# Kernel tuning notes

Hardware: AMD Instinct MI355X
Metric: run time of the kernel (lower is better)

Reference implementation:

```python
import jax, jax.numpy as jnp
import numpy as np

TEMPERATURE = 0.5
EPS = 1e-12  # F.normalize eps


def setup_inputs() -> dict:
    key = jax.random.key(0)
    z = jax.random.normal(key, (2048, 8, 256), dtype=jnp.float32)
    return {"z": z}


def reference(z):
    B, D = z.shape[0], z.shape[1]
    z = z.reshape(B, D, -1)  # [B, D, F]
    # F.normalize along features
    norm = jnp.linalg.norm(z, axis=-1, keepdims=True)
    zn = z / jnp.maximum(norm, EPS)

    # Positive term: per sample b, sim among D views -> [B, D, D], off-diagonal sum
    sim_pos = jnp.exp(jnp.einsum('bdf,bef->bde', zn, zn) / TEMPERATURE)
    eye_d = jnp.eye(D, dtype=bool)
    pos = jnp.sum(jnp.where(eye_d[None], 0.0, sim_pos), axis=(1, 2))  # [B]

    # Negative term: per view d, sim among B samples -> [D, B, B], row-wise off-diag mean, summed over views
    sim_neg = jnp.exp(jnp.einsum('bdf,cdf->dbc', zn, zn) / TEMPERATURE)
    eye_b = jnp.eye(B, dtype=bool)
    neg = jnp.sum(jnp.where(eye_b[None], 0.0, sim_neg), axis=-1) / (B - 1)  # [D, B]
    neg = jnp.sum(neg, axis=0)  # [B]

    logits = pos / (pos + neg)  # [B]
    # torch CrossEntropyLoss(reduction='sum') with 1-D input [C] and float target ones(C):
    # loss = -sum_c target_c * log_softmax(logits)_c = -sum(log_softmax(logits))
    error = -jnp.sum(jax.nn.log_softmax(logits))
    return error / B
```

## Files before the change

kernel.cpp:

```cpp
#include <hip/hip_runtime.h>
#include <hip/hip_bf16.h>

#define B_N 2048
#define D_V 8
#define F_D 256
#define TILE 128
#define BC 64
#define LSTR 264

#define SCALE_F 1.69864364f

#if defined(__has_builtin)
#  if __has_builtin(__builtin_amdgcn_exp2f)
#    define EXP2F(x) __builtin_amdgcn_exp2f(x)
#  else
#    define EXP2F(x) exp2f(x)
#  endif
#else
#  define EXP2F(x) exp2f(x)
#endif

typedef __attribute__((ext_vector_type(8))) short short8;
typedef __attribute__((ext_vector_type(4))) float floatx4;

__device__ inline unsigned short f2bf(float f) {
    __hip_bfloat16 h = __float2bfloat16(f);
    return *reinterpret_cast<unsigned short*>(&h);
}

__device__ inline float wave_reduce_sum(float v) {
    #pragma unroll
    for (int off = 1; off < 64; off <<= 1)
        v += __shfl_xor(v, off, 64);
    return v;
}

__device__ inline float wave_reduce_max(float v) {
    #pragma unroll
    for (int off = 1; off < 64; off <<= 1)
        v = fmaxf(v, __shfl_xor(v, off, 64));
    return v;
}

__global__ __launch_bounds__(256)
void np_kernel(const float* __restrict__ z, unsigned short* __restrict__ zn,
               float* __restrict__ ns8, float* __restrict__ pos) {
    __shared__ __align__(16) unsigned short Zs[32 * LSTR];
    int tid = threadIdx.x;
    int gid = blockIdx.x * 256 + tid;
    if (gid < D_V * B_N) ns8[gid] = 0.0f;

    int w = tid >> 6, lane = tid & 63;
    int b = blockIdx.x * 4 + w;
    #pragma unroll
    for (int k = 0; k < 8; k++) {
        const float4 v = ((const float4*)(z + ((size_t)b * 8 + k) * F_D))[lane];
        float ss = v.x * v.x + v.y * v.y + v.z * v.z + v.w * v.w;
        ss = wave_reduce_sum(ss);
        float inv = SCALE_F / fmaxf(sqrtf(ss), 1e-12f);
        ushort4 o;
        o.x = f2bf(v.x * inv);
        o.y = f2bf(v.y * inv);
        o.z = f2bf(v.z * inv);
        o.w = f2bf(v.w * inv);
        ((ushort4*)(zn + (size_t)k * (B_N * F_D) + (size_t)b * F_D))[lane] = o;
        *(ushort4*)(&Zs[(w * 8 + k) * LSTR + lane * 4]) = o;
    }
    __syncthreads();

    if (w < 2) {
        int q = lane >> 4, li = lane & 15;
        int lr = (w * 2 + (li >> 3)) * 8 + (li & 7);
        short8 a[8];
        #pragma unroll
        for (int kk = 0; kk < 8; kk++)
            a[kk] = *(const short8*)(&Zs[lr * LSTR + kk * 32 + q * 8]);
        floatx4 acc = {0.f, 0.f, 0.f, 0.f};
        #pragma unroll
        for (int kk = 0; kk < 8; kk++)
            acc = __builtin_amdgcn_mfma_f32_16x16x32_bf16(a[kk], a[kk], acc, 0, 0, 0);
        float p0 = 0.f, p1 = 0.f;
        #pragma unroll
        for (int r = 0; r < 4; r++) {
            int row = q * 4 + r, col = li;
            bool same_sample = (row >> 3) == (col >> 3);
            if (same_sample && row != col) {
                float e = EXP2F(acc[r]);
                if (row < 8) p0 += e; else p1 += e;
            }
        }
        p0 = wave_reduce_sum(p0);
        p1 = wave_reduce_sum(p1);
        if (lane == 0) {
            int s0 = blockIdx.x * 4 + w * 2;
            pos[s0] = p0;
            pos[s0 + 1] = p1;
        }
    }
}

__global__ __launch_bounds__(512)
void neg_kernel(const unsigned short* __restrict__ zn,
                float* __restrict__ ns8) {
    __shared__ __align__(16) unsigned short Bs[BC * LSTR];
    const int bid = blockIdx.x;
    const int d = bid & 7;
    int trem = bid >> 3;
    int i = 0;
    while (trem >= 16 - i) { trem -= 16 - i; ++i; }
    const int j = i + trem;
    const bool diag = (i == j);
    const unsigned short* Z = zn + (size_t)d * (B_N * F_D);
    int tid = threadIdx.x, w = tid >> 6, lane = tid & 63;
    int q = lane >> 4, li = lane & 15;
    int r0 = i * TILE + w * 16;
    const int jc = j * TILE;

    short8 a[8];
    #pragma unroll
    for (int kk = 0; kk < 8; kk++)
        a[kk] = *(const short8*)(Z + (size_t)(r0 + li) * F_D + kk * 32 + q * 8);

    short8 breg[4];
    #pragma unroll
    for (int it = 0; it < 4; ++it) {
        int idx = it * 512 + tid;
        int row = idx >> 5, kc = idx & 31;
        breg[it] = *(const short8*)(Z + (size_t)(jc + row) * F_D + kc * 8);
    }
    #pragma unroll
    for (int it = 0; it < 4; ++it) {
        int idx = it * 512 + tid;
        int row = idx >> 5, kc = idx & 31;
        *(short8*)(&Bs[row * LSTR + kc * 8]) = breg[it];
    }
    #pragma unroll
    for (int it = 0; it < 4; ++it) {
        int idx = it * 512 + tid;
        int row = idx >> 5, kc = idx & 31;
        breg[it] = *(const short8*)(Z + (size_t)(jc + BC + row) * F_D + kc * 8);
    }

    float rs[4] = {0.f, 0.f, 0.f, 0.f};
    float cs[8];

    __syncthreads();

    #pragma unroll
    for (int stage = 0; stage < 2; ++stage) {
        #pragma unroll
        for (int ct = 0; ct < 4; ++ct) {
            const unsigned short* bp = &Bs[(ct * 16 + li) * LSTR + q * 8];
            floatx4 acc = {0.f, 0.f, 0.f, 0.f};
            #pragma unroll
            for (int kk = 0; kk < 8; kk++) {
                short8 bf = *(const short8*)(bp + kk * 32);
                acc = __builtin_amdgcn_mfma_f32_16x16x32_bf16(a[kk], bf, acc, 0, 0, 0);
            }
            int gcol = jc + stage * BC + ct * 16 + li;
            float csum = 0.f;
            #pragma unroll
            for (int r = 0; r < 4; r++) {
                float e = EXP2F(acc[r]);
                if (diag) {
                    int grow = r0 + q * 4 + r;
                    if (grow == gcol) e = 0.f;
                }
                rs[r] += e;
                csum += e;
            }
            csum += __shfl_xor(csum, 16, 64);
            csum += __shfl_xor(csum, 32, 64);
            cs[stage * 4 + ct] = csum;
        }
        if (stage == 0) {
            __syncthreads();
            #pragma unroll
            for (int it = 0; it < 4; ++it) {
                int idx = it * 512 + tid;
                int row = idx >> 5, kc = idx & 31;
                *(short8*)(&Bs[row * LSTR + kc * 8]) = breg[it];
            }
            __syncthreads();
        }
    }

    #pragma unroll
    for (int off = 1; off < 16; off <<= 1)
        #pragma unroll
        for (int r = 0; r < 4; r++)
            rs[r] += __shfl_xor(rs[r], off, 64);
    {
        float rv = 0.f;
        #pragma unroll
        for (int r = 0; r < 4; r++)
            if (li == r) rv = rs[r];
        if (li < 4)
            atomicAdd(&ns8[d * B_N + r0 + q * 4 + li], rv);
    }

    if (!diag) {
        float v0 = 0.f, v1 = 0.f;
        #pragma unroll
        for (int c = 0; c < 4; c++)
            if (q == c) { v0 = cs[c]; v1 = cs[c + 4]; }
        atomicAdd(&ns8[d * B_N + jc + q * 16 + li], v0);
        atomicAdd(&ns8[d * B_N + jc + 64 + q * 16 + li], v1);
    }
}

__global__ void final_kernel(const float* __restrict__ pos,
                             const float* __restrict__ ns8,
                             float* __restrict__ out) {
    __shared__ float redm[4], reds[4], redl[4];
    int t = threadIdx.x, w = t >> 6, lane = t & 63;
    float vals[8];
    float lmax = -1e30f;
    #pragma unroll
    for (int i = 0; i < 8; i++) {
        int idx = t * 8 + i;
        float nsum = 0.f;
        #pragma unroll
        for (int d = 0; d < D_V; d++) nsum += ns8[d * B_N + idx];
        float p = pos[idx];
        float l = p / (p + nsum * (1.0f / (float)(B_N - 1)));
        vals[i] = l;
        lmax = fmaxf(lmax, l);
    }
    lmax = wave_reduce_max(lmax);
    if (lane == 0) redm[w] = lmax;
    __syncthreads();
    float m = fmaxf(fmaxf(redm[0], redm[1]), fmaxf(redm[2], redm[3]));
    float se = 0.f, sl = 0.f;
    #pragma unroll
    for (int i = 0; i < 8; i++) { se += expf(vals[i] - m); sl += vals[i]; }
    se = wave_reduce_sum(se);
    sl = wave_reduce_sum(sl);
    if (lane == 0) { reds[w] = se; redl[w] = sl; }
    __syncthreads();
    if (t == 0) {
        float S = reds[0] + reds[1] + reds[2] + reds[3];
        float L = redl[0] + redl[1] + redl[2] + redl[3];
        out[0] = m + logf(S) - L * (1.0f / (float)B_N);
    }
}

extern "C" void kernel_launch(void* const* d_in, const int* in_sizes, int n_in,
                              void* d_out, int out_size, void* d_ws, size_t ws_size,
                              hipStream_t stream) {
    const float* z = (const float*)d_in[0];
    float* out = (float*)d_out;
    unsigned short* zn = (unsigned short*)d_ws;
    float* ns8 = (float*)((char*)d_ws + (size_t)D_V * B_N * F_D * 2);
    float* pos = ns8 + D_V * B_N;

    np_kernel<<<dim3(512), 256, 0, stream>>>(z, zn, ns8, pos);
    neg_kernel<<<dim3(136 * 8), 512, 0, stream>>>(zn, ns8);
    final_kernel<<<1, 256, 0, stream>>>(pos, ns8, out);
}
```

Baseline: 86.80 us.

## Split neg tiles into row halves and double-buffer B staging in LDS

Each 128x128 tile of the negative-similarity kernel is now handled by two 256-thread blocks, one per 64-row half. The B columns are streamed in four 32-row stages through a two-slot LDS buffer, which needs only one barrier per stage and overlaps the global prefetch with MFMA work. This doubles the number of blocks and lowers LDS use per block, aiming at better occupancy and latency hiding. In exchange, each B tile is loaded twice from global/L2 and twice as many column-sum atomics are issued.

```diff
diff --git a/kernel.cpp b/kernel.cpp
--- a/kernel.cpp
+++ b/kernel.cpp
@@ -5,7 +5,7 @@
 #define D_V 8
 #define F_D 256
 #define TILE 128
-#define BC 64
+#define BC 32
 #define LSTR 264
 
 #define SCALE_F 1.69864364f
@@ -99,13 +99,15 @@
     }
 }
 
-__global__ __launch_bounds__(512)
+__global__ __launch_bounds__(256)
 void neg_kernel(const unsigned short* __restrict__ zn,
                 float* __restrict__ ns8) {
-    __shared__ __align__(16) unsigned short Bs[BC * LSTR];
+    __shared__ __align__(16) unsigned short Bs[2][BC * LSTR];
     const int bid = blockIdx.x;
     const int d = bid & 7;
-    int trem = bid >> 3;
+    int rest = bid >> 3;
+    const int half = rest & 1;
+    int trem = rest >> 1;
     int i = 0;
     while (trem >= 16 - i) { trem -= 16 - i; ++i; }
     const int j = i + trem;
@@ -113,7 +115,7 @@
     const unsigned short* Z = zn + (size_t)d * (B_N * F_D);
     int tid = threadIdx.x, w = tid >> 6, lane = tid & 63;
     int q = lane >> 4, li = lane & 15;
-    int r0 = i * TILE + w * 16;
+    int r0 = i * TILE + half * 64 + w * 16;
     const int jc = j * TILE;
 
     short8 a[8];
@@ -124,19 +126,19 @@
     short8 breg[4];
     #pragma unroll
     for (int it = 0; it < 4; ++it) {
-        int idx = it * 512 + tid;
+        int idx = it * 256 + tid;
         int row = idx >> 5, kc = idx & 31;
         breg[it] = *(const short8*)(Z + (size_t)(jc + row) * F_D + kc * 8);
     }
     #pragma unroll
     for (int it = 0; it < 4; ++it) {
-        int idx = it * 512 + tid;
+        int idx = it * 256 + tid;
         int row = idx >> 5, kc = idx & 31;
-        *(short8*)(&Bs[row * LSTR + kc * 8]) = breg[it];
+        *(short8*)(&Bs[0][row * LSTR + kc * 8]) = breg[it];
     }
     #pragma unroll
     for (int it = 0; it < 4; ++it) {
-        int idx = it * 512 + tid;
+        int idx = it * 256 + tid;
         int row = idx >> 5, kc = idx & 31;
         breg[it] = *(const short8*)(Z + (size_t)(jc + BC + row) * F_D + kc * 8);
     }
@@ -147,17 +149,18 @@
     __syncthreads();
 
     #pragma unroll
-    for (int stage = 0; stage < 2; ++stage) {
-        #pragma unroll
-        for (int ct = 0; ct < 4; ++ct) {
-            const unsigned short* bp = &Bs[(ct * 16 + li) * LSTR + q * 8];
+    for (int st = 0; st < 4; ++st) {
+        #pragma unroll
+        for (int ct = 0; ct < 2; ++ct) {
+            const unsigned short* bp = &Bs[st & 1][(ct * 16 + li) * LSTR + q * 8];
             floatx4 acc = {0.f, 0.f, 0.f, 0.f};
             #pragma unroll
             for (int kk = 0; kk < 8; kk++) {
                 short8 bf = *(const short8*)(bp + kk * 32);
                 acc = __builtin_amdgcn_mfma_f32_16x16x32_bf16(a[kk], bf, acc, 0, 0, 0);
             }
-            int gcol = jc + stage * BC + ct * 16 + li;
+            const int g = st * 2 + ct;
+            int gcol = jc + g * 16 + li;
             float csum = 0.f;
             #pragma unroll
             for (int r = 0; r < 4; r++) {
@@ -171,18 +174,25 @@
             }
             csum += __shfl_xor(csum, 16, 64);
             csum += __shfl_xor(csum, 32, 64);
-            cs[stage * 4 + ct] = csum;
-        }
-        if (stage == 0) {
-            __syncthreads();
+            cs[g] = csum;
+        }
+        if (st < 3) {
             #pragma unroll
             for (int it = 0; it < 4; ++it) {
-                int idx = it * 512 + tid;
+                int idx = it * 256 + tid;
                 int row = idx >> 5, kc = idx & 31;
-                *(short8*)(&Bs[row * LSTR + kc * 8]) = breg[it];
-            }
-            __syncthreads();
-        }
+                *(short8*)(&Bs[(st + 1) & 1][row * LSTR + kc * 8]) = breg[it];
+            }
+        }
+        if (st < 2) {
+            #pragma unroll
+            for (int it = 0; it < 4; ++it) {
+                int idx = it * 256 + tid;
+                int row = idx >> 5, kc = idx & 31;
+                breg[it] = *(const short8*)(Z + (size_t)(jc + (st + 2) * BC + row) * F_D + kc * 8);
+            }
+        }
+        if (st < 3) __syncthreads();
     }
 
     #pragma unroll
@@ -255,6 +265,6 @@
     float* pos = ns8 + D_V * B_N;
 
     np_kernel<<<dim3(512), 256, 0, stream>>>(z, zn, ns8, pos);
-    neg_kernel<<<dim3(136 * 8), 512, 0, stream>>>(zn, ns8);
+    neg_kernel<<<dim3(136 * 2 * 8), 256, 0, stream>>>(zn, ns8);
     final_kernel<<<1, 256, 0, stream>>>(pos, ns8, out);
 }
```

Measured after the change: 86.60 us. No clear change (-0.2%).
